# Performance work log

Measured on AMD Instinct MI355X. Metric: run time of the kernel, lower is better.

The kernel has to match this reference:

```python
import jax, jax.numpy as jnp
import numpy as np

B, S, E, H = 2, 2048, 1024, 16
D = E // H  # head_dim = 64


def _rope_angles(seq_len, d, dtype=jnp.float32):
    # standard RoPE frequencies: theta_i = 10000^{-2i/d}
    inv_freq = 1.0 / (10000.0 ** (jnp.arange(0, d, 2, dtype=dtype) / d))  # [d/2]
    pos = jnp.arange(seq_len, dtype=dtype)                                # [S]
    ang = pos[:, None] * inv_freq[None, :]                                # [S, d/2]
    ang = jnp.concatenate([ang, ang], axis=-1)                            # [S, d]
    return jnp.cos(ang), jnp.sin(ang)


def _rotate_half(t):
    t1, t2 = jnp.split(t, 2, axis=-1)
    return jnp.concatenate([-t2, t1], axis=-1)


def _apply_rope(t, cos, sin):
    # t: [B, H, S, D]; cos/sin: [S, D]
    return t * cos[None, None, :, :] + _rotate_half(t) * sin[None, None, :, :]


def setup_inputs() -> dict:
    key = jax.random.key(0)
    ks = jax.random.split(key, 6)
    x = jax.random.normal(ks[0], (B, S, E), dtype=jnp.float32)
    mask = jnp.tril(jnp.ones((S, S), dtype=bool))  # causal: True = attend
    scale = 1.0 / np.sqrt(E)
    Wq = jax.random.normal(ks[1], (E, E), dtype=jnp.float32) * scale
    Wk = jax.random.normal(ks[2], (E, E), dtype=jnp.float32) * scale
    Wv = jax.random.normal(ks[3], (E, E), dtype=jnp.float32) * scale
    Wo = jax.random.normal(ks[4], (E, E), dtype=jnp.float32) * scale
    z = jnp.zeros((E,), dtype=jnp.float32)
    return {"x": x, "mask": mask, "Wq": Wq, "bq": z, "Wk": Wk, "bk": z,
            "Wv": Wv, "bv": z, "Wo": Wo, "bo": z}


def reference(x, mask, Wq, bq, Wk, bk, Wv, bv, Wo, bo):
    b, s, e = x.shape
    # QKV projections (nn.Linear convention: y = x @ W.T + b)
    def proj(W, bias):
        y = jnp.einsum('bse,fe->bsf', x, W) + bias
        return y.reshape(b, s, H, D).transpose(0, 2, 1, 3)  # [B,H,S,D]
    q, k, v = proj(Wq, bq), proj(Wk, bk), proj(Wv, bv)
    # RoPE on q and k (per-head rotary over head_dim)
    cos, sin = _rope_angles(s, D, dtype=x.dtype)
    q = _apply_rope(q, cos, sin)
    k = _apply_rope(k, cos, sin)
    # SDPA with boolean mask (True = attend)
    scores = jnp.einsum('bhqd,bhkd->bhqk', q, k) / jnp.sqrt(jnp.asarray(D, x.dtype))
    neg = jnp.asarray(jnp.finfo(x.dtype).min, x.dtype)
    scores = jnp.where(mask[None, None, :, :], scores, neg)
    attn = jax.nn.softmax(scores, axis=-1)
    out = jnp.einsum('bhqk,bhkd->bhqd', attn, v)          # [B,H,S,D]
    out = out.transpose(0, 2, 1, 3).reshape(b, s, e)       # [B,S,E]
    return jnp.einsum('bse,fe->bsf', out, Wo) + bo
```

## Files before the change

kernel.cpp:

```cpp
#include <hip/hip_runtime.h>
#include <hip/hip_bf16.h>

typedef unsigned short u16;
typedef unsigned int u32;
typedef __bf16 bf16x8 __attribute__((ext_vector_type(8)));
typedef float f32x4 __attribute__((ext_vector_type(4)));

#define S_LEN 2048
#define NHEAD 16
#define HDIM  64
#define EMB   1024
#define BATCH 2

__device__ __forceinline__ float bf2f(u16 u) {
  union { unsigned int i; float f; } c; c.i = ((unsigned int)u) << 16; return c.f;
}
__device__ __forceinline__ u16 f2bf(float f) {
  union { float f; unsigned int i; } c; c.f = f;
  unsigned int i = c.i;
  return (u16)((i + 0x7FFFu + ((i >> 16) & 1u)) >> 16);
}
__device__ __forceinline__ u16 f2bf_trunc(float f) {
  union { float f; unsigned int i; } c; c.f = f;
  return (u16)(c.i >> 16);
}
__device__ __forceinline__ f32x4 mfma16(bf16x8 a, bf16x8 b, f32x4 c) {
  return __builtin_amdgcn_mfma_f32_16x16x32_bf16(a, b, c, 0, 0, 0);
}

__global__ __launch_bounds__(256) void convert_kernel(
    const void* __restrict__ x, const void* __restrict__ Wq,
    const void* __restrict__ Wk, const void* __restrict__ Wv,
    const void* __restrict__ Wo,
    u16* __restrict__ xb, u16* __restrict__ wqb, u16* __restrict__ wkb,
    u16* __restrict__ wvb, u16* __restrict__ wob,
    int* __restrict__ flag, float2* __restrict__ tab)
{
  __shared__ int s_flag;
  if (threadIdx.x == 0) s_flag = 0;
  __syncthreads();
  {
    const u16* xs = (const u16*)x;
    u16 w0 = xs[threadIdx.x * 2], w1 = xs[threadIdx.x * 2 + 1];
    if ((((w0 >> 7) & 0xFF) >= 0xC0) || (((w1 >> 7) & 0xFF) >= 0xC0))
      atomicOr(&s_flag, 1);
  }
  __syncthreads();
  const int f32io = s_flag;
  if (blockIdx.x == 0 && threadIdx.x == 0) flag[0] = f32io;

  size_t gid = (size_t)blockIdx.x * 256 + threadIdx.x;
  size_t e = gid * 8;
  const void* src; u16* dst; size_t off;
  if (e < 4194304) { src = x; dst = xb; off = e; }
  else {
    size_t rr = e - 4194304;
    int j = (int)(rr >> 20); off = rr & 1048575;
    src = (j == 0) ? Wq : (j == 1) ? Wk : (j == 2) ? Wv : Wo;
    dst = (j == 0) ? wqb : (j == 1) ? wkb : (j == 2) ? wvb : wob;
  }
  if (f32io) {
    const float* s = (const float*)src + off;
    float4 a = *(const float4*)s;
    float4 b2 = *(const float4*)(s + 4);
    ushort4 u0; u0.x = f2bf(a.x); u0.y = f2bf(a.y); u0.z = f2bf(a.z); u0.w = f2bf(a.w);
    ushort4 u1; u1.x = f2bf(b2.x); u1.y = f2bf(b2.y); u1.z = f2bf(b2.z); u1.w = f2bf(b2.w);
    *(ushort4*)(dst + off) = u0;
    *(ushort4*)(dst + off + 4) = u1;
  } else {
    *(uint4*)(dst + off) = *(const uint4*)((const u16*)src + off);
  }

  if (blockIdx.x < 256) {
    int id = blockIdx.x * 256 + threadIdx.x;
    int s = id >> 5, i = id & 31;
    float f = exp2f(-(float)i * 0.41524101186092029f);
    float ang = (float)s * f;
    tab[id] = make_float2(cosf(ang), sinf(ang));
  }
}

__device__ __forceinline__ void gemm_core_pipe(
    const u16* __restrict__ A, const u16* __restrict__ W,
    int m0, int n0, int t, f32x4 (&acc)[4][4],
    u16* __restrict__ Ash, u16* __restrict__ Bsh)
{
  const int lane = t & 63, lr = lane & 15, quad = lane >> 4;
  const int wv = t >> 6;
  const int wm = (wv & 1) * 64, wn = (wv >> 1) * 64;
  const int i0 = t, i1 = t + 256;
  const u16* gA0 = A + (size_t)(m0 + (i0 >> 2)) * 1024 + (i0 & 3) * 8;
  const u16* gA1 = A + (size_t)(m0 + (i1 >> 2)) * 1024 + (i1 & 3) * 8;
  const u16* gB0 = W + (size_t)(n0 + (i0 >> 2)) * 1024 + (i0 & 3) * 8;
  const u16* gB1 = W + (size_t)(n0 + (i1 >> 2)) * 1024 + (i1 & 3) * 8;
  uint4 ra0 = *(const uint4*)gA0;
  uint4 ra1 = *(const uint4*)gA1;
  uint4 rb0 = *(const uint4*)gB0;
  uint4 rb1 = *(const uint4*)gB1;
  for (int kt = 0; kt < 1024; kt += 32) {
    __syncthreads();
    *(uint4*)(Ash + (size_t)i0 * 8) = ra0;
    *(uint4*)(Ash + (size_t)i1 * 8) = ra1;
    *(uint4*)(Bsh + (size_t)i0 * 8) = rb0;
    *(uint4*)(Bsh + (size_t)i1 * 8) = rb1;
    __syncthreads();
    if (kt + 32 < 1024) {
      ra0 = *(const uint4*)(gA0 + kt + 32);
      ra1 = *(const uint4*)(gA1 + kt + 32);
      rb0 = *(const uint4*)(gB0 + kt + 32);
      rb1 = *(const uint4*)(gB1 + kt + 32);
    }
    bf16x8 af[4], bfr[4];
#pragma unroll
    for (int mi = 0; mi < 4; ++mi)
      af[mi] = *(const bf16x8*)(Ash + (size_t)(wm + mi * 16 + lr) * 32 + quad * 8);
#pragma unroll
    for (int ni = 0; ni < 4; ++ni)
      bfr[ni] = *(const bf16x8*)(Bsh + (size_t)(wn + ni * 16 + lr) * 32 + quad * 8);
#pragma unroll
    for (int mi = 0; mi < 4; ++mi)
#pragma unroll
      for (int ni = 0; ni < 4; ++ni)
        acc[mi][ni] = mfma16(af[mi], bfr[ni], acc[mi][ni]);
  }
}

__device__ __forceinline__ void gemm_epilogue(
    int mode, int f32io, f32x4 (&acc)[4][4],
    const void* biasvp, void* outvp, int m0, int n0, int t,
    const float2* __restrict__ tab)
{
  const int lane = t & 63, lr = lane & 15, quad = lane >> 4;
  const int wv = t >> 6;
  const int wm = (wv & 1) * 64, wn = (wv >> 1) * 64;
  const float* biasf = (const float*)biasvp;
  const u16* biasb = (const u16*)biasvp;
#define BIASV(n) (f32io ? biasf[(n)] : bf2f(biasb[(n)]))
  if (mode == 1) {
    u16* Out = (u16*)outvp;
#pragma unroll
    for (int mi = 0; mi < 4; ++mi) {
#pragma unroll
      for (int r = 0; r < 4; ++r) {
        int mm = m0 + wm + mi * 16 + quad * 4 + r;
        int s = mm & (S_LEN - 1), b = mm >> 11;
        float2 cs0 = tab[s * 32 + lr];
        float2 cs1 = tab[s * 32 + 16 + lr];
#pragma unroll
        for (int ni = 0; ni < 4; ++ni) {
          int n = n0 + wn + ni * 16 + lr;
          int h = n >> 6, d = n & 63;
          float v  = acc[mi][ni][r]     + BIASV(n);
          float vp = acc[mi][ni ^ 2][r] + BIASV(n ^ 32);
          float rot = (d < 32) ? -vp : vp;
          float cc = (ni & 1) ? cs1.x : cs0.x;
          float ss = (ni & 1) ? cs1.y : cs0.y;
          size_t off = (((size_t)(b * NHEAD + h)) * S_LEN + s) * HDIM + d;
          Out[off] = f2bf(v * cc + rot * ss);
        }
      }
    }
  } else if (mode == 2) {
    u16* Out = (u16*)outvp;
#pragma unroll
    for (int mi = 0; mi < 4; ++mi) {
      int mm = m0 + wm + mi * 16 + quad * 4;
      int s = mm & (S_LEN - 1), b = mm >> 11;
#pragma unroll
      for (int ni = 0; ni < 4; ++ni) {
        int n = n0 + wn + ni * 16 + lr;
        int h = n >> 6, d = n & 63;
        float bv = BIASV(n);
        u16 p0 = f2bf(acc[mi][ni][0] + bv);
        u16 p1 = f2bf(acc[mi][ni][1] + bv);
        u16 p2 = f2bf(acc[mi][ni][2] + bv);
        u16 p3 = f2bf(acc[mi][ni][3] + bv);
        uint2 pk = make_uint2((u32)p0 | ((u32)p1 << 16),
                              (u32)p2 | ((u32)p3 << 16));
        size_t off = (((size_t)(b * NHEAD + h)) * HDIM + d) * S_LEN + s;
        *(uint2*)(Out + off) = pk;
      }
    }
  }
#undef BIASV
}

__global__ __launch_bounds__(256) void gemm_qkv(
    const u16* __restrict__ A, const u16* __restrict__ Wq,
    const u16* __restrict__ Wk, const u16* __restrict__ Wv,
    const void* bq, const void* bk, const void* bv,
    u16* qo, u16* ko, u16* vo, const int* __restrict__ dflag,
    const float2* __restrict__ tab)
{
  alignas(16) __shared__ u16 Ash[128 * 32];
  alignas(16) __shared__ u16 Bsh[128 * 32];
  const int wsel = blockIdx.x >> 3;
  const u16* W = (wsel == 0) ? Wq : (wsel == 1) ? Wk : Wv;
  const void* bias = (wsel == 0) ? bq : (wsel == 1) ? bk : bv;
  void* out = (wsel == 0) ? (void*)qo : (wsel == 1) ? (void*)ko : (void*)vo;
  const int mode = (wsel == 2) ? 2 : 1;
  const int m0 = blockIdx.y * 128, n0 = (blockIdx.x & 7) * 128;
  f32x4 acc[4][4];
  const f32x4 zero4 = {0.f, 0.f, 0.f, 0.f};
#pragma unroll
  for (int i = 0; i < 4; ++i)
#pragma unroll
    for (int j = 0; j < 4; ++j) acc[i][j] = zero4;
  gemm_core_pipe(A, W, m0, n0, threadIdx.x, acc, Ash, Bsh);
  gemm_epilogue(mode, dflag[0], acc, bias, out, m0, n0, threadIdx.x, tab);
}

__global__ __launch_bounds__(256) void gemm_out(
    const u16* __restrict__ A, const u16* __restrict__ W,
    const void* bias, void* out, const int* __restrict__ dflag)
{
  alignas(16) __shared__ u16 Ash[64 * 32];
  alignas(16) __shared__ u16 Bsh[128 * 32];
  const int t = threadIdx.x, lane = t & 63, wv = t >> 6;
  const int lr = lane & 15, quad = lane >> 4;
  const int m0 = blockIdx.y * 64, n0 = blockIdx.x * 128;
  const int wm = (wv & 1) * 32, wn = (wv >> 1) * 64;
  const int f32io = dflag[0];
  const int i0 = t, i1 = t + 256;
  const u16* gA0 = A + (size_t)(m0 + (i0 >> 2)) * 1024 + (i0 & 3) * 8;
  const u16* gB0 = W + (size_t)(n0 + (i0 >> 2)) * 1024 + (i0 & 3) * 8;
  const u16* gB1 = W + (size_t)(n0 + (i1 >> 2)) * 1024 + (i1 & 3) * 8;
  uint4 ra0 = *(const uint4*)gA0;
  uint4 rb0 = *(const uint4*)gB0;
  uint4 rb1 = *(const uint4*)gB1;

  f32x4 acc[2][4];
  const f32x4 zero4 = {0.f, 0.f, 0.f, 0.f};
#pragma unroll
  for (int i = 0; i < 2; ++i)
#pragma unroll
    for (int j = 0; j < 4; ++j) acc[i][j] = zero4;

  for (int kt = 0; kt < 1024; kt += 32) {
    __syncthreads();
    *(uint4*)(Ash + (size_t)i0 * 8) = ra0;
    *(uint4*)(Bsh + (size_t)i0 * 8) = rb0;
    *(uint4*)(Bsh + (size_t)i1 * 8) = rb1;
    __syncthreads();
    if (kt + 32 < 1024) {
      ra0 = *(const uint4*)(gA0 + kt + 32);
      rb0 = *(const uint4*)(gB0 + kt + 32);
      rb1 = *(const uint4*)(gB1 + kt + 32);
    }
    bf16x8 af[2], bfr[4];
#pragma unroll
    for (int mi = 0; mi < 2; ++mi)
      af[mi] = *(const bf16x8*)(Ash + (size_t)(wm + mi * 16 + lr) * 32 + quad * 8);
#pragma unroll
    for (int ni = 0; ni < 4; ++ni)
      bfr[ni] = *(const bf16x8*)(Bsh + (size_t)(wn + ni * 16 + lr) * 32 + quad * 8);
#pragma unroll
    for (int mi = 0; mi < 2; ++mi)
#pragma unroll
      for (int ni = 0; ni < 4; ++ni)
        acc[mi][ni] = mfma16(af[mi], bfr[ni], acc[mi][ni]);
  }

  const float* biasf = (const float*)bias;
  const u16* biasb = (const u16*)bias;
  float* Outf = (float*)out;
  u16* Outb = (u16*)out;
#pragma unroll
  for (int mi = 0; mi < 2; ++mi) {
#pragma unroll
    for (int r = 0; r < 4; ++r) {
      int mm = m0 + wm + mi * 16 + quad * 4 + r;
#pragma unroll
      for (int ni = 0; ni < 4; ++ni) {
        int n = n0 + wn + ni * 16 + lr;
        float bv = f32io ? biasf[n] : bf2f(biasb[n]);
        float v = acc[mi][ni][r] + bv;
        size_t off = (size_t)mm * 1024 + n;
        if (f32io) Outf[off] = v; else Outb[off] = f2bf(v);
      }
    }
  }
}

__device__ __forceinline__ void attn_phase(
    const bf16x8 (&qf)[2], f32x4 (&oacc)[4], float (&lsum)[4],
    u16 (&Ksh)[64][72], u16 (&Vsh)[64][72], u16 (&Psh)[8][16][72],
    int kv0, int q0w, bool diag, int lr, int quad, int wv)
{
  const f32x4 zero4 = {0.f, 0.f, 0.f, 0.f};
  f32x4 sc[4];
#pragma unroll
  for (int ni = 0; ni < 4; ++ni) {
    bf16x8 kf0 = *(const bf16x8*)&Ksh[ni * 16 + lr][quad * 8];
    bf16x8 kf1 = *(const bf16x8*)&Ksh[ni * 16 + lr][32 + quad * 8];
    f32x4 z = zero4;
    z = mfma16(qf[0], kf0, z);
    z = mfma16(qf[1], kf1, z);
    sc[ni] = z;
  }
  if (diag) {
#pragma unroll
    for (int ni = 0; ni < 4; ++ni)
#pragma unroll
      for (int r = 0; r < 4; ++r) {
        float sarg = sc[ni][r] * 0.18033688f - 21.64042561f;
        if (kv0 + ni * 16 + lr > q0w + quad * 4 + r) sarg = -1e4f;
        float p = exp2f(sarg);
        sc[ni][r] = p;
        lsum[r] += p;
      }
  } else {
#pragma unroll
    for (int ni = 0; ni < 4; ++ni)
#pragma unroll
      for (int r = 0; r < 4; ++r) {
        float p = exp2f(sc[ni][r] * 0.18033688f - 21.64042561f);
        sc[ni][r] = p;
        lsum[r] += p;
      }
  }
#pragma unroll
  for (int ni = 0; ni < 4; ++ni)
#pragma unroll
    for (int r = 0; r < 4; ++r)
      Psh[wv][quad * 4 + r][ni * 16 + lr] = f2bf_trunc(sc[ni][r]);
  bf16x8 pa0 = *(const bf16x8*)&Psh[wv][lr][quad * 8];
  bf16x8 pa1 = *(const bf16x8*)&Psh[wv][lr][32 + quad * 8];
#pragma unroll
  for (int oni = 0; oni < 4; ++oni) {
    bf16x8 vf0 = *(const bf16x8*)&Vsh[oni * 16 + lr][quad * 8];
    bf16x8 vf1 = *(const bf16x8*)&Vsh[oni * 16 + lr][32 + quad * 8];
    oacc[oni] = mfma16(pa0, vf0, oacc[oni]);
    oacc[oni] = mfma16(pa1, vf1, oacc[oni]);
  }
}

__device__ __forceinline__ void attn_finish(
    f32x4 (&oacc)[4], float (&lsum)[4], u16* __restrict__ O,
    int bh, int q0w, int lr, int quad)
{
  const int b = bh >> 4, h = bh & 15;
#pragma unroll
  for (int r = 0; r < 4; ++r) {
#pragma unroll
    for (int off = 1; off < 16; off <<= 1) lsum[r] += __shfl_xor(lsum[r], off);
    lsum[r] = 1.f / lsum[r];
  }
#pragma unroll
  for (int oni = 0; oni < 4; ++oni)
#pragma unroll
    for (int r = 0; r < 4; ++r) {
      int s = q0w + quad * 4 + r;
      int e = h * HDIM + oni * 16 + lr;
      O[((size_t)(b * S_LEN + s)) * EMB + e] = f2bf(oacc[oni][r] * lsum[r]);
    }
}

__global__ __launch_bounds__(512) void attn_kernel(
    const u16* __restrict__ Q, const u16* __restrict__ Kr,
    const u16* __restrict__ Vt, u16* __restrict__ O)
{
  alignas(16) __shared__ u16 Ksh[64][72];
  alignas(16) __shared__ u16 Vsh[64][72];
  alignas(16) __shared__ u16 Psh[8][16][72];
  const int t = threadIdx.x, lane = t & 63, wv = t >> 6;
  const int lr = lane & 15, quad = lane >> 4;
  const int bh = blockIdx.y;
  const int qtA = blockIdx.x;
  const int qtB = 31 - qtA;
  const int myTile = (wv < 4) ? qtA : qtB;
  const int q0w = myTile * 64 + (wv & 3) * 16;
  const size_t base = (size_t)bh * S_LEN * HDIM;

  bf16x8 qf[2];
  {
    const u16* qrow = Q + base + (size_t)(q0w + lr) * HDIM + quad * 8;
    qf[0] = *(const bf16x8*)qrow;
    qf[1] = *(const bf16x8*)(qrow + 32);
  }

  f32x4 oacc[4];
  float lsum[4];
  const f32x4 zero4 = {0.f, 0.f, 0.f, 0.f};
#pragma unroll
  for (int i = 0; i < 4; ++i) { oacc[i] = zero4; lsum[i] = 0.f; }

  const int jmax = qtB;
  for (int j = 0; j <= jmax; ++j) {
    const int kv0 = j * 64;
    __syncthreads();
    {
      int r = t >> 3, cc = (t & 7) * 8;
      *(uint4*)&Ksh[r][cc] = *(const uint4*)(Kr + base + (size_t)(kv0 + r) * HDIM + cc);
      *(uint4*)&Vsh[r][cc] = *(const uint4*)(Vt + base + (size_t)r * S_LEN + kv0 + cc);
    }
    __syncthreads();
    if (j <= myTile)
      attn_phase(qf, oacc, lsum, Ksh, Vsh, Psh, kv0, q0w, j == myTile, lr, quad, wv);
  }

  attn_finish(oacc, lsum, O, bh, q0w, lr, quad);
}

extern "C" void kernel_launch(void* const* d_in, const int* in_sizes, int n_in,
                              void* d_out, int out_size, void* d_ws, size_t ws_size,
                              hipStream_t stream) {
  const void* x  = d_in[0];
  const void* Wq = d_in[2]; const void* bq = d_in[3];
  const void* Wk = d_in[4]; const void* bk = d_in[5];
  const void* Wv = d_in[6]; const void* bv = d_in[7];
  const void* Wo = d_in[8]; const void* bo = d_in[9];

  char* ws = (char*)d_ws;
  int* flag = (int*)ws;
  u16* xb  = (u16*)(ws + 256);
  u16* qws = xb  + 4194304;
  u16* kws = qws + 4194304;
  u16* vws = kws + 4194304;
  u16* wqb = vws + 4194304;
  u16* wkb = wqb + 1048576;
  u16* wvb = wkb + 1048576;
  u16* wob = wvb + 1048576;
  float2* tab = (float2*)(wob + 1048576);
  u16* ows = xb;

  convert_kernel<<<4096, 256, 0, stream>>>(x, Wq, Wk, Wv, Wo,
                                           xb, wqb, wkb, wvb, wob, flag, tab);
  gemm_qkv<<<dim3(24, 32), 256, 0, stream>>>(xb, wqb, wkb, wvb,
                                             bq, bk, bv, qws, kws, vws, flag, tab);
  attn_kernel<<<dim3(16, 32), 512, 0, stream>>>(qws, kws, vws, ows);
  gemm_out<<<dim3(8, 64), 256, 0, stream>>>(ows, wob, bo, d_out, flag);
}
```

Measured before the change: 240.3 us.

## Double-buffer GEMM tiles via direct global-to-LDS loads and prefetch attention K/V

The QKV and output-projection GEMMs now use two LDS buffers per operand, filled with global_load_lds builtins that copy global memory straight into shared memory. Each iteration issues the next tile's load before the MFMAs on the current tile, and only one barrier per iteration is kept. The attention kernel prefetches the next K/V tile into registers while the current tile is processed. The aim is to hide global-load latency behind compute and remove register staging and a barrier. In exchange LDS use doubles, and correctness relies on the wave-uniform LDS base addressing of global_load_lds matching the previous tile layout.

```diff
diff --git a/kernel.cpp b/kernel.cpp
--- a/kernel.cpp
+++ b/kernel.cpp
@@ -26,6 +26,11 @@
 }
 __device__ __forceinline__ f32x4 mfma16(bf16x8 a, bf16x8 b, f32x4 c) {
   return __builtin_amdgcn_mfma_f32_16x16x32_bf16(a, b, c, 0, 0, 0);
+}
+__device__ __forceinline__ void cp16(const u16* g, u16* l) {
+  __builtin_amdgcn_global_load_lds(
+      (const __attribute__((address_space(1))) u32*)g,
+      (__attribute__((address_space(3))) u32*)l, 16, 0, 0);
 }
 
 __global__ __launch_bounds__(256) void convert_kernel(
@@ -80,7 +85,7 @@
   }
 }
 
-__device__ __forceinline__ void gemm_core_pipe(
+__device__ __forceinline__ void gemm_core_db(
     const u16* __restrict__ A, const u16* __restrict__ W,
     int m0, int n0, int t, f32x4 (&acc)[4][4],
     u16* __restrict__ Ash, u16* __restrict__ Bsh)
@@ -88,40 +93,42 @@
   const int lane = t & 63, lr = lane & 15, quad = lane >> 4;
   const int wv = t >> 6;
   const int wm = (wv & 1) * 64, wn = (wv >> 1) * 64;
-  const int i0 = t, i1 = t + 256;
-  const u16* gA0 = A + (size_t)(m0 + (i0 >> 2)) * 1024 + (i0 & 3) * 8;
-  const u16* gA1 = A + (size_t)(m0 + (i1 >> 2)) * 1024 + (i1 & 3) * 8;
-  const u16* gB0 = W + (size_t)(n0 + (i0 >> 2)) * 1024 + (i0 & 3) * 8;
-  const u16* gB1 = W + (size_t)(n0 + (i1 >> 2)) * 1024 + (i1 & 3) * 8;
-  uint4 ra0 = *(const uint4*)gA0;
-  uint4 ra1 = *(const uint4*)gA1;
-  uint4 rb0 = *(const uint4*)gB0;
-  uint4 rb1 = *(const uint4*)gB1;
+  const int r0 = t >> 2, c0 = (t & 3) * 8;
+  const int r1 = (t + 256) >> 2, c1 = (t & 3) * 8;
+  const int lds0 = (t & 192) * 8;
+  const int lds1 = (256 + (t & 192)) * 8;
+  const u16* gA0 = A + (size_t)(m0 + r0) * 1024 + c0;
+  const u16* gA1 = A + (size_t)(m0 + r1) * 1024 + c1;
+  const u16* gB0 = W + (size_t)(n0 + r0) * 1024 + c0;
+  const u16* gB1 = W + (size_t)(n0 + r1) * 1024 + c1;
+
+  cp16(gA0, Ash + lds0); cp16(gA1, Ash + lds1);
+  cp16(gB0, Bsh + lds0); cp16(gB1, Bsh + lds1);
+  __syncthreads();
+
   for (int kt = 0; kt < 1024; kt += 32) {
-    __syncthreads();
-    *(uint4*)(Ash + (size_t)i0 * 8) = ra0;
-    *(uint4*)(Ash + (size_t)i1 * 8) = ra1;
-    *(uint4*)(Bsh + (size_t)i0 * 8) = rb0;
-    *(uint4*)(Bsh + (size_t)i1 * 8) = rb1;
-    __syncthreads();
+    const int cur = (kt >> 5) & 1;
+    const u16* Ac = Ash + cur * 4096;
+    const u16* Bc = Bsh + cur * 4096;
+    bf16x8 af[4], bfr[4];
+#pragma unroll
+    for (int mi = 0; mi < 4; ++mi)
+      af[mi] = *(const bf16x8*)(Ac + (wm + mi * 16 + lr) * 32 + quad * 8);
+#pragma unroll
+    for (int ni = 0; ni < 4; ++ni)
+      bfr[ni] = *(const bf16x8*)(Bc + (wn + ni * 16 + lr) * 32 + quad * 8);
     if (kt + 32 < 1024) {
-      ra0 = *(const uint4*)(gA0 + kt + 32);
-      ra1 = *(const uint4*)(gA1 + kt + 32);
-      rb0 = *(const uint4*)(gB0 + kt + 32);
-      rb1 = *(const uint4*)(gB1 + kt + 32);
-    }
-    bf16x8 af[4], bfr[4];
-#pragma unroll
-    for (int mi = 0; mi < 4; ++mi)
-      af[mi] = *(const bf16x8*)(Ash + (size_t)(wm + mi * 16 + lr) * 32 + quad * 8);
-#pragma unroll
-    for (int ni = 0; ni < 4; ++ni)
-      bfr[ni] = *(const bf16x8*)(Bsh + (size_t)(wn + ni * 16 + lr) * 32 + quad * 8);
+      u16* An = Ash + (1 - cur) * 4096;
+      u16* Bn = Bsh + (1 - cur) * 4096;
+      cp16(gA0 + kt + 32, An + lds0); cp16(gA1 + kt + 32, An + lds1);
+      cp16(gB0 + kt + 32, Bn + lds0); cp16(gB1 + kt + 32, Bn + lds1);
+    }
 #pragma unroll
     for (int mi = 0; mi < 4; ++mi)
 #pragma unroll
       for (int ni = 0; ni < 4; ++ni)
         acc[mi][ni] = mfma16(af[mi], bfr[ni], acc[mi][ni]);
+    __syncthreads();
   }
 }
 
@@ -192,8 +199,8 @@
     u16* qo, u16* ko, u16* vo, const int* __restrict__ dflag,
     const float2* __restrict__ tab)
 {
-  alignas(16) __shared__ u16 Ash[128 * 32];
-  alignas(16) __shared__ u16 Bsh[128 * 32];
+  alignas(16) __shared__ u16 Ash[2 * 128 * 32];
+  alignas(16) __shared__ u16 Bsh[2 * 128 * 32];
   const int wsel = blockIdx.x >> 3;
   const u16* W = (wsel == 0) ? Wq : (wsel == 1) ? Wk : Wv;
   const void* bias = (wsel == 0) ? bq : (wsel == 1) ? bk : bv;
@@ -206,7 +213,7 @@
   for (int i = 0; i < 4; ++i)
 #pragma unroll
     for (int j = 0; j < 4; ++j) acc[i][j] = zero4;
-  gemm_core_pipe(A, W, m0, n0, threadIdx.x, acc, Ash, Bsh);
+  gemm_core_db(A, W, m0, n0, threadIdx.x, acc, Ash, Bsh);
   gemm_epilogue(mode, dflag[0], acc, bias, out, m0, n0, threadIdx.x, tab);
 }
 
@@ -214,20 +221,21 @@
     const u16* __restrict__ A, const u16* __restrict__ W,
     const void* bias, void* out, const int* __restrict__ dflag)
 {
-  alignas(16) __shared__ u16 Ash[64 * 32];
-  alignas(16) __shared__ u16 Bsh[128 * 32];
+  alignas(16) __shared__ u16 Ash[2 * 64 * 32];
+  alignas(16) __shared__ u16 Bsh[2 * 128 * 32];
   const int t = threadIdx.x, lane = t & 63, wv = t >> 6;
   const int lr = lane & 15, quad = lane >> 4;
   const int m0 = blockIdx.y * 64, n0 = blockIdx.x * 128;
   const int wm = (wv & 1) * 32, wn = (wv >> 1) * 64;
   const int f32io = dflag[0];
-  const int i0 = t, i1 = t + 256;
-  const u16* gA0 = A + (size_t)(m0 + (i0 >> 2)) * 1024 + (i0 & 3) * 8;
-  const u16* gB0 = W + (size_t)(n0 + (i0 >> 2)) * 1024 + (i0 & 3) * 8;
-  const u16* gB1 = W + (size_t)(n0 + (i1 >> 2)) * 1024 + (i1 & 3) * 8;
-  uint4 ra0 = *(const uint4*)gA0;
-  uint4 rb0 = *(const uint4*)gB0;
-  uint4 rb1 = *(const uint4*)gB1;
+
+  const int r0 = t >> 2, c0 = (t & 3) * 8;
+  const int r1 = (t + 256) >> 2;
+  const int lds0 = (t & 192) * 8;
+  const int lds1 = (256 + (t & 192)) * 8;
+  const u16* gA0 = A + (size_t)(m0 + (r0 & 63)) * 1024 + c0;
+  const u16* gB0 = W + (size_t)(n0 + r0) * 1024 + c0;
+  const u16* gB1 = W + (size_t)(n0 + r1) * 1024 + c0;
 
   f32x4 acc[2][4];
   const f32x4 zero4 = {0.f, 0.f, 0.f, 0.f};
@@ -236,29 +244,33 @@
 #pragma unroll
     for (int j = 0; j < 4; ++j) acc[i][j] = zero4;
 
+  cp16(gA0, Ash + lds0);
+  cp16(gB0, Bsh + lds0); cp16(gB1, Bsh + lds1);
+  __syncthreads();
+
   for (int kt = 0; kt < 1024; kt += 32) {
-    __syncthreads();
-    *(uint4*)(Ash + (size_t)i0 * 8) = ra0;
-    *(uint4*)(Bsh + (size_t)i0 * 8) = rb0;
-    *(uint4*)(Bsh + (size_t)i1 * 8) = rb1;
-    __syncthreads();
+    const int cur = (kt >> 5) & 1;
+    const u16* Ac = Ash + cur * 2048;
+    const u16* Bc = Bsh + cur * 4096;
+    bf16x8 af[2], bfr[4];
+#pragma unroll
+    for (int mi = 0; mi < 2; ++mi)
+      af[mi] = *(const bf16x8*)(Ac + (wm + mi * 16 + lr) * 32 + quad * 8);
+#pragma unroll
+    for (int ni = 0; ni < 4; ++ni)
+      bfr[ni] = *(const bf16x8*)(Bc + (wn + ni * 16 + lr) * 32 + quad * 8);
     if (kt + 32 < 1024) {
-      ra0 = *(const uint4*)(gA0 + kt + 32);
-      rb0 = *(const uint4*)(gB0 + kt + 32);
-      rb1 = *(const uint4*)(gB1 + kt + 32);
-    }
-    bf16x8 af[2], bfr[4];
-#pragma unroll
-    for (int mi = 0; mi < 2; ++mi)
-      af[mi] = *(const bf16x8*)(Ash + (size_t)(wm + mi * 16 + lr) * 32 + quad * 8);
-#pragma unroll
-    for (int ni = 0; ni < 4; ++ni)
-      bfr[ni] = *(const bf16x8*)(Bsh + (size_t)(wn + ni * 16 + lr) * 32 + quad * 8);
+      u16* An = Ash + (1 - cur) * 2048;
+      u16* Bn = Bsh + (1 - cur) * 4096;
+      cp16(gA0 + kt + 32, An + lds0);
+      cp16(gB0 + kt + 32, Bn + lds0); cp16(gB1 + kt + 32, Bn + lds1);
+    }
 #pragma unroll
     for (int mi = 0; mi < 2; ++mi)
 #pragma unroll
       for (int ni = 0; ni < 4; ++ni)
         acc[mi][ni] = mfma16(af[mi], bfr[ni], acc[mi][ni]);
+    __syncthreads();
   }
 
   const float* biasf = (const float*)bias;
@@ -385,18 +397,23 @@
 #pragma unroll
   for (int i = 0; i < 4; ++i) { oacc[i] = zero4; lsum[i] = 0.f; }
 
+  const int rr = t >> 3, cc = (t & 7) * 8;
+  uint4 krg = *(const uint4*)(Kr + base + (size_t)rr * HDIM + cc);
+  uint4 vrg = *(const uint4*)(Vt + base + (size_t)rr * S_LEN + cc);
+
   const int jmax = qtB;
   for (int j = 0; j <= jmax; ++j) {
-    const int kv0 = j * 64;
     __syncthreads();
-    {
-      int r = t >> 3, cc = (t & 7) * 8;
-      *(uint4*)&Ksh[r][cc] = *(const uint4*)(Kr + base + (size_t)(kv0 + r) * HDIM + cc);
-      *(uint4*)&Vsh[r][cc] = *(const uint4*)(Vt + base + (size_t)r * S_LEN + kv0 + cc);
-    }
+    *(uint4*)&Ksh[rr][cc] = krg;
+    *(uint4*)&Vsh[rr][cc] = vrg;
     __syncthreads();
+    if (j < jmax) {
+      const int kv1 = (j + 1) * 64;
+      krg = *(const uint4*)(Kr + base + (size_t)(kv1 + rr) * HDIM + cc);
+      vrg = *(const uint4*)(Vt + base + (size_t)rr * S_LEN + kv1 + cc);
+    }
     if (j <= myTile)
-      attn_phase(qf, oacc, lsum, Ksh, Vsh, Psh, kv0, q0w, j == myTile, lr, quad, wv);
+      attn_phase(qf, oacc, lsum, Ksh, Vsh, Psh, j * 64, q0w, j == myTile, lr, quad, wv);
   }
 
   attn_finish(oacc, lsum, O, bh, q0w, lr, quad);
```

Result: faster. 212.5 us (-11.6%).
